# Kernel tuning notes

Hardware: AMD Instinct MI355X
Metric: run time of the kernel (lower is better)

The kernel has to match this reference:

```python
import jax, jax.numpy as jnp
import numpy as np

N_NODES = 100000
N_EDGES = 1600000
NEG_SLOPE = 0.2
EPS = 1e-16


def gat_conv(x, edge_index, W, att_src, att_dst, bias, heads, out_ch, concat):
    # x: [N, F_in]; edge_index: [2, E] with edge (src j -> dst i)
    N = x.shape[0]
    src, dst = edge_index[0], edge_index[1]
    h = (x @ W).reshape(N, heads, out_ch)              # [N, H, C]
    a_src = (h * att_src[None]).sum(-1)                # [N, H]
    a_dst = (h * att_dst[None]).sum(-1)                # [N, H]
    e = a_src[src] + a_dst[dst]                        # [E, H]
    e = jnp.where(e > 0, e, NEG_SLOPE * e)             # LeakyReLU(0.2)
    # segment softmax over destination node
    m = jax.ops.segment_max(e, dst, num_segments=N)    # [N, H]
    m = jnp.where(jnp.isfinite(m), m, 0.0)
    ex = jnp.exp(e - m[dst])                           # [E, H]
    s = jax.ops.segment_sum(ex, dst, num_segments=N)   # [N, H]
    alpha = ex / (s[dst] + EPS)                        # [E, H]
    msg = h[src] * alpha[..., None]                    # [E, H, C]
    out = jax.ops.segment_sum(msg, dst, num_segments=N)  # [N, H, C]
    if concat:
        out = out.reshape(N, heads * out_ch)
    else:
        out = out.mean(axis=1)
    return out + bias


def setup_inputs() -> dict:
    key = jax.random.key(0)
    ks = jax.random.split(key, 8)
    x = jax.random.normal(ks[0], (N_NODES, 2), dtype=jnp.float32)
    edge_index = jax.random.randint(ks[1], (2, N_EDGES), 0, N_NODES, dtype=jnp.int64)
    glorot = lambda k, shape, fan: jax.random.normal(k, shape, jnp.float32) * (1.0 / np.sqrt(fan))
    W1 = glorot(ks[2], (2, 128), 2)
    att_src1 = glorot(ks[3], (8, 16), 16)
    att_dst1 = glorot(ks[4], (8, 16), 16)
    b1 = jnp.zeros((128,), jnp.float32)
    W2 = glorot(ks[5], (128, 4), 128)
    att_src2 = glorot(ks[6], (1, 4), 4)
    att_dst2 = glorot(ks[7], (1, 4), 4)
    b2 = jnp.zeros((4,), jnp.float32)
    return {"x": x, "edge_index": edge_index, "W1": W1, "att_src1": att_src1,
            "att_dst1": att_dst1, "b1": b1, "W2": W2, "att_src2": att_src2,
            "att_dst2": att_dst2, "b2": b2}


def reference(x, edge_index, W1, att_src1, att_dst1, b1, W2, att_src2, att_dst2, b2):
    h = gat_conv(x, edge_index, W1, att_src1, att_dst1, b1, heads=8, out_ch=16, concat=True)
    h = jax.nn.relu(h)
    # dropout p=0.6 is identity in eval mode
    h = gat_conv(h, edge_index, W2, att_src2, att_dst2, b2, heads=1, out_ch=4, concat=True)
    return jax.nn.log_softmax(h, axis=1)
```

## Files before the change

kernel.cpp:

```cpp
#include <hip/hip_runtime.h>
#include <math.h>

static constexpr float kNegSlope = 0.2f;
static constexpr float kEps = 1e-16f;
static constexpr int SLICES = 256;
static constexpr int BSHIFT = 6;
static constexpr int BMASK = 63;
static constexpr unsigned SRCMASK = 0x1FFFFu;
static constexpr int CAP = 1536;

__device__ __forceinline__ float leaky(float v) {
    return v > 0.0f ? v : kNegSlope * v;
}


__global__ __launch_bounds__(512) void k_hist1(const int* __restrict__ ei,
                                               int* __restrict__ table,
                                               int* __restrict__ rowptr,
                                               int E, int N, int NBUCK) {
    __shared__ int hist[1664];
    int b = blockIdx.x, t = threadIdx.x;
    if (b == 0 && t == 0) rowptr[N] = E;
    for (int i = t; i < NBUCK; i += 512) hist[i] = 0;
    __syncthreads();
    int S = (((E + SLICES - 1) / SLICES) + 3) & ~3;
    int lo = b * S, hi = min(lo + S, E);
    for (int i = lo + t * 4; i < hi; i += 512 * 4) {
        int4 dv = *(const int4*)(ei + E + i);
        atomicAdd(&hist[dv.x >> BSHIFT], 1);
        atomicAdd(&hist[dv.y >> BSHIFT], 1);
        atomicAdd(&hist[dv.z >> BSHIFT], 1);
        atomicAdd(&hist[dv.w >> BSHIFT], 1);
    }
    __syncthreads();
    for (int i = t; i < NBUCK; i += 512) table[i * SLICES + b] = hist[i];
}

__global__ __launch_bounds__(256) void k_scan_reduce(const int* __restrict__ src,
                                                     int* __restrict__ partial, int n) {
    __shared__ int wsum[4];
    int b = blockIdx.x, t = threadIdx.x;
    int base = b * 1024 + t * 4;
    int s = 0;
#pragma unroll
    for (int k = 0; k < 4; ++k) {
        int idx = base + k;
        s += (idx < n) ? src[idx] : 0;
    }
#pragma unroll
    for (int off = 1; off < 64; off <<= 1) s += __shfl_xor(s, off);
    if ((t & 63) == 0) wsum[t >> 6] = s;
    __syncthreads();
    if (t == 0) partial[b] = wsum[0] + wsum[1] + wsum[2] + wsum[3];
}

__global__ __launch_bounds__(256) void k_scan_apply(int* __restrict__ data,
                                                    const int* __restrict__ partial,
                                                    int n, int nsb) {
    __shared__ int sm[8];
    __shared__ int baseSh;
    int b = blockIdx.x, t = threadIdx.x;
    int acc = 0;
    for (int i = t; i < b; i += 256) acc += partial[i];
#pragma unroll
    for (int off = 1; off < 64; off <<= 1) acc += __shfl_xor(acc, off);
    if ((t & 63) == 0) sm[t >> 6] = acc;
    __syncthreads();
    if (t == 0) baseSh = sm[0] + sm[1] + sm[2] + sm[3];
    __syncthreads();
    int chunkBase = baseSh;
    __syncthreads();
    int base = b * 1024 + t * 4;
    int v[4];
#pragma unroll
    for (int k = 0; k < 4; ++k) {
        int idx = base + k;
        v[k] = (idx < n) ? data[idx] : 0;
    }
    int sum4 = v[0] + v[1] + v[2] + v[3];
    int s = sum4;
#pragma unroll
    for (int off = 1; off < 64; off <<= 1) {
        int u = __shfl_up(s, off);
        if ((t & 63) >= off) s += u;
    }
    if ((t & 63) == 63) sm[t >> 6] = s;
    __syncthreads();
    int woff = 0;
    int w = t >> 6;
    for (int ww = 0; ww < w; ++ww) woff += sm[ww];
    int ex = chunkBase + woff + (s - sum4);
#pragma unroll
    for (int k = 0; k < 4; ++k) {
        int idx = base + k;
        if (idx < n) data[idx] = ex;
        ex += v[k];
    }
}

__global__ __launch_bounds__(512) void k_bin2(const int* __restrict__ ei,
                                              const int* __restrict__ table,
                                              unsigned* __restrict__ sbuf, int E, int NBUCK) {
    __shared__ int cur[1664];
    int b = blockIdx.x, t = threadIdx.x;
    for (int i = t; i < NBUCK; i += 512) cur[i] = table[i * SLICES + b];
    __syncthreads();
    int S = (((E + SLICES - 1) / SLICES) + 3) & ~3;
    int lo = b * S, hi = min(lo + S, E);
    for (int i = lo + t * 4; i < hi; i += 512 * 4) {
        int4 sv = *(const int4*)(ei + i);
        int4 dv = *(const int4*)(ei + E + i);
        int pos;
        pos = atomicAdd(&cur[dv.x >> BSHIFT], 1);
        sbuf[pos] = (unsigned)sv.x | ((unsigned)(dv.x & BMASK) << 17);
        pos = atomicAdd(&cur[dv.y >> BSHIFT], 1);
        sbuf[pos] = (unsigned)sv.y | ((unsigned)(dv.y & BMASK) << 17);
        pos = atomicAdd(&cur[dv.z >> BSHIFT], 1);
        sbuf[pos] = (unsigned)sv.z | ((unsigned)(dv.z & BMASK) << 17);
        pos = atomicAdd(&cur[dv.w >> BSHIFT], 1);
        sbuf[pos] = (unsigned)sv.w | ((unsigned)(dv.w & BMASK) << 17);
    }
}

__global__ __launch_bounds__(512, 4) void k_bfinal_g1(
        const unsigned* __restrict__ sbuf, const int* __restrict__ table,
        int* __restrict__ rowptr, int* __restrict__ ssrc,
        const float* __restrict__ x,
        const float* __restrict__ W1, const float* __restrict__ att_src1,
        const float* __restrict__ att_dst1, const float* __restrict__ b1,
        const float* __restrict__ W2, float* __restrict__ h2,
        int N, int E, int NBUCK) {
    __shared__ int hist[64];
    __shared__ int excl[64];
    __shared__ int cur[64];
    __shared__ int sl[CAP];
    __shared__ float pbuf[32];
    int b = blockIdx.x;
    int t = threadIdx.x;
    int lo = table[b * SLICES];
    int hi = (b + 1 < NBUCK) ? table[(b + 1) * SLICES] : E;
    int cnt = hi - lo;
    bool inLds = (cnt <= CAP);

    if (t < 64) hist[t] = 0;
    if (t >= 64 && t < 96) {
        int u = t - 64;
        int which = u >> 4;
        int hd = u & 15;
        int h = hd >> 1, d = hd & 1;
        const float* att = which ? att_dst1 : att_src1;
        float s = 0.0f;
#pragma unroll
        for (int c = 0; c < 16; ++c) s += W1[d * 128 + h * 16 + c] * att[h * 16 + c];
        pbuf[which * 16 + d * 8 + h] = s;
    }
    __syncthreads();

    for (int i = lo + t; i < hi; i += 512) atomicAdd(&hist[sbuf[i] >> 17], 1);
    __syncthreads();

    if (t < 64) {
        int own = hist[t];
        int v = own;
#pragma unroll
        for (int off = 1; off < 64; off <<= 1) {
            int u = __shfl_up(v, off);
            if (t >= off) v += u;
        }
        excl[t] = v - own;
        cur[t] = v - own;
        int node = (b << BSHIFT) + t;
        if (node < N) rowptr[node] = lo + (v - own);
    }
    __syncthreads();

    if (inLds) {
        for (int i = lo + t; i < hi; i += 512) {
            unsigned v = sbuf[i];
            int pos = atomicAdd(&cur[v >> 17], 1);
            sl[pos] = (int)(v & SRCMASK);
        }
        __syncthreads();
        for (int i = t; i < cnt; i += 512) ssrc[lo + i] = sl[i];
    } else {
        for (int i = lo + t; i < hi; i += 512) {
            unsigned v = sbuf[i];
            int pos = atomicAdd(&cur[v >> 17], 1);
            ssrc[lo + pos] = (int)(v & SRCMASK);
        }
        __syncthreads();
    }
    __syncthreads();

    int dl = t >> 3, q = t & 7;
    int node = (b << BSHIFT) + dl;
    int st = excl[dl];
    int ecnt = hist[dl];
    float2 xn = ((const float2*)x)[min(node, N - 1)];
    float Ps0[8], Ps1[8], adv[8], l[8], s0[8], s1[8];
#pragma unroll
    for (int h = 0; h < 8; ++h) {
        Ps0[h] = pbuf[h];
        Ps1[h] = pbuf[8 + h];
        adv[h] = xn.x * pbuf[16 + h] + xn.y * pbuf[24 + h];
        l[h] = 0.f; s0[h] = 0.f; s1[h] = 0.f;
    }
    if (inLds) {
        for (int j = q; j < ecnt; j += 8) {
            int src = sl[st + j];
            float2 xs = ((const float2*)x)[src];
#pragma unroll
            for (int h = 0; h < 8; ++h) {
                float p = __expf(leaky(xs.x * Ps0[h] + xs.y * Ps1[h] + adv[h]));
                l[h] += p; s0[h] += p * xs.x; s1[h] += p * xs.y;
            }
        }
    } else {
        for (int j = q; j < ecnt; j += 8) {
            int src = ssrc[lo + st + j];
            float2 xs = ((const float2*)x)[src];
#pragma unroll
            for (int h = 0; h < 8; ++h) {
                float p = __expf(leaky(xs.x * Ps0[h] + xs.y * Ps1[h] + adv[h]));
                l[h] += p; s0[h] += p * xs.x; s1[h] += p * xs.y;
            }
        }
    }
#pragma unroll
    for (int off = 1; off < 8; off <<= 1) {
#pragma unroll
        for (int h = 0; h < 8; ++h) {
            l[h] += __shfl_xor(l[h], off);
            s0[h] += __shfl_xor(s0[h], off);
            s1[h] += __shfl_xor(s1[h], off);
        }
    }
    float h0 = 0.f, h1v = 0.f, h2v = 0.f, h3 = 0.f;
    {
        float inv = 1.0f / (l[q] + kEps);
        float sX0 = s0[q] * inv, sX1 = s1[q] * inv;
#pragma unroll
        for (int c = 0; c < 16; ++c) {
            int col = q * 16 + c;
            float o = fmaxf(W1[col] * sX0 + W1[128 + col] * sX1 + b1[col], 0.0f);
            h0 += o * W2[col * 4 + 0];
            h1v += o * W2[col * 4 + 1];
            h2v += o * W2[col * 4 + 2];
            h3 += o * W2[col * 4 + 3];
        }
    }
#pragma unroll
    for (int off = 1; off < 8; off <<= 1) {
        h0 += __shfl_xor(h0, off);
        h1v += __shfl_xor(h1v, off);
        h2v += __shfl_xor(h2v, off);
        h3 += __shfl_xor(h3, off);
    }
    if (node < N && q == 0) {
        ((float4*)h2)[node] = make_float4(h0, h1v, h2v, h3);
    }
}

__global__ __launch_bounds__(256) void k_gather2_out(
        const int* __restrict__ rowptr, const int* __restrict__ ssrc,
        const float* __restrict__ h2, const float* __restrict__ att_src2,
        const float* __restrict__ att_dst2, const float* __restrict__ b2,
        float* __restrict__ out, int N) {
    int idx = blockIdx.x * blockDim.x + threadIdx.x;
    int n = idx >> 3, q = idx & 7;
    if (n >= N) return;
    int start = rowptr[n], end = rowptr[n + 1];
    float4 as2 = *(const float4*)att_src2;
    float4 ad2v = *(const float4*)att_dst2;
    float4 hn = ((const float4*)h2)[n];
    float ad = hn.x * ad2v.x + hn.y * ad2v.y + hn.z * ad2v.z + hn.w * ad2v.w;
    float l = 0.0f;
    float4 acc = make_float4(0.f, 0.f, 0.f, 0.f);
    for (int j = start + q; j < end; j += 8) {
        int src = ssrc[j];
        float4 hv = ((const float4*)h2)[src];
        float e = hv.x * as2.x + hv.y * as2.y + hv.z * as2.z + hv.w * as2.w + ad;
        float p = __expf(leaky(e));
        l += p;
        acc.x += p * hv.x; acc.y += p * hv.y; acc.z += p * hv.z; acc.w += p * hv.w;
    }
#pragma unroll
    for (int off = 1; off < 8; off <<= 1) {
        l += __shfl_xor(l, off);
        acc.x += __shfl_xor(acc.x, off);
        acc.y += __shfl_xor(acc.y, off);
        acc.z += __shfl_xor(acc.z, off);
        acc.w += __shfl_xor(acc.w, off);
    }
    if (q == 0) {
        float inv = 1.0f / (l + kEps);
        float4 v = make_float4(acc.x * inv + b2[0], acc.y * inv + b2[1],
                               acc.z * inv + b2[2], acc.w * inv + b2[3]);
        float mx = fmaxf(fmaxf(v.x, v.y), fmaxf(v.z, v.w));
        float sum = __expf(v.x - mx) + __expf(v.y - mx) + __expf(v.z - mx) + __expf(v.w - mx);
        float lse = mx + logf(sum);
        ((float4*)out)[n] = make_float4(v.x - lse, v.y - lse, v.z - lse, v.w - lse);
    }
}

extern "C" void kernel_launch(void* const* d_in, const int* in_sizes, int n_in,
                              void* d_out, int out_size, void* d_ws, size_t ws_size,
                              hipStream_t stream) {
    const float* x        = (const float*)d_in[0];
    const int*   ei       = (const int*)d_in[1];
    const float* W1       = (const float*)d_in[2];
    const float* att_src1 = (const float*)d_in[3];
    const float* att_dst1 = (const float*)d_in[4];
    const float* b1       = (const float*)d_in[5];
    const float* W2       = (const float*)d_in[6];
    const float* att_src2 = (const float*)d_in[7];
    const float* att_dst2 = (const float*)d_in[8];
    const float* b2       = (const float*)d_in[9];

    const int N = in_sizes[0] / 2;
    const int E = in_sizes[1] / 2;
    const int NBUCK = (N + BMASK) >> BSHIFT;
    const int ntable = NBUCK * SLICES;
    const int nsb = (ntable + 1023) / 1024;

    int* table     = (int*)d_ws;
    int* partial   = table + ntable + 64;
    int* rowptr    = partial + 1024;
    int* ssrc      = rowptr + ((N + 4) & ~3);
    unsigned* sbuf = (unsigned*)(ssrc + E);
    float* h2      = (float*)(sbuf + E);

    k_hist1<<<SLICES, 512, 0, stream>>>(ei, table, rowptr, E, N, NBUCK);
    k_scan_reduce<<<nsb, 256, 0, stream>>>(table, partial, ntable);
    k_scan_apply<<<nsb, 256, 0, stream>>>(table, partial, ntable, nsb);
    k_bin2<<<SLICES, 512, 0, stream>>>(ei, table, sbuf, E, NBUCK);

    k_bfinal_g1<<<NBUCK, 512, 0, stream>>>(sbuf, table, rowptr, ssrc, x,
                                           W1, att_src1, att_dst1, b1, W2, h2,
                                           N, E, NBUCK);

    k_gather2_out<<<(N * 8 + 255) / 256, 256, 0, stream>>>(rowptr, ssrc, h2,
                                                           att_src2, att_dst2, b2,
                                                           (float*)d_out, N);
}
```

Before: 174.3 us.

## Carry gathered source features through binning to avoid random x loads

The binning kernel now gathers each edge's source node features x[src] and writes them next to the packed src/dst word, so the per-bucket kernel reads contiguous features instead of doing random gathers. The bucket kernel stages both raw words and features in LDS, sorts them together, and reads features from LDS in the attention loop. The random gather moves into the binning pass, where it costs extra scattered 8-byte writes, and LDS use per block grows to about 30KB, which may reduce occupancy.

```diff
diff --git a/kernel.cpp b/kernel.cpp
--- a/kernel.cpp
+++ b/kernel.cpp
@@ -100,30 +100,39 @@
 
 __global__ __launch_bounds__(512) void k_bin2(const int* __restrict__ ei,
                                               const int* __restrict__ table,
-                                              unsigned* __restrict__ sbuf, int E, int NBUCK) {
+                                              const float* __restrict__ x,
+                                              unsigned* __restrict__ sbufs,
+                                              float2* __restrict__ sbufx,
+                                              int E, int NBUCK) {
     __shared__ int cur[1664];
     int b = blockIdx.x, t = threadIdx.x;
     for (int i = t; i < NBUCK; i += 512) cur[i] = table[i * SLICES + b];
     __syncthreads();
     int S = (((E + SLICES - 1) / SLICES) + 3) & ~3;
     int lo = b * S, hi = min(lo + S, E);
+    const float2* x2 = (const float2*)x;
     for (int i = lo + t * 4; i < hi; i += 512 * 4) {
         int4 sv = *(const int4*)(ei + i);
         int4 dv = *(const int4*)(ei + E + i);
         int pos;
         pos = atomicAdd(&cur[dv.x >> BSHIFT], 1);
-        sbuf[pos] = (unsigned)sv.x | ((unsigned)(dv.x & BMASK) << 17);
+        sbufs[pos] = (unsigned)sv.x | ((unsigned)(dv.x & BMASK) << 17);
+        sbufx[pos] = x2[sv.x];
         pos = atomicAdd(&cur[dv.y >> BSHIFT], 1);
-        sbuf[pos] = (unsigned)sv.y | ((unsigned)(dv.y & BMASK) << 17);
+        sbufs[pos] = (unsigned)sv.y | ((unsigned)(dv.y & BMASK) << 17);
+        sbufx[pos] = x2[sv.y];
         pos = atomicAdd(&cur[dv.z >> BSHIFT], 1);
-        sbuf[pos] = (unsigned)sv.z | ((unsigned)(dv.z & BMASK) << 17);
+        sbufs[pos] = (unsigned)sv.z | ((unsigned)(dv.z & BMASK) << 17);
+        sbufx[pos] = x2[sv.z];
         pos = atomicAdd(&cur[dv.w >> BSHIFT], 1);
-        sbuf[pos] = (unsigned)sv.w | ((unsigned)(dv.w & BMASK) << 17);
+        sbufs[pos] = (unsigned)sv.w | ((unsigned)(dv.w & BMASK) << 17);
+        sbufx[pos] = x2[sv.w];
     }
 }
 
 __global__ __launch_bounds__(512, 4) void k_bfinal_g1(
-        const unsigned* __restrict__ sbuf, const int* __restrict__ table,
+        const unsigned* __restrict__ sbufs, const float2* __restrict__ sbufx,
+        const int* __restrict__ table,
         int* __restrict__ rowptr, int* __restrict__ ssrc,
         const float* __restrict__ x,
         const float* __restrict__ W1, const float* __restrict__ att_src1,
@@ -133,7 +142,10 @@
     __shared__ int hist[64];
     __shared__ int excl[64];
     __shared__ int cur[64];
-    __shared__ int sl[CAP];
+    __shared__ unsigned raws[CAP];
+    __shared__ float2 rawx[CAP];
+    __shared__ float2 slx[CAP];
+    __shared__ int sls[CAP];
     __shared__ float pbuf[32];
     int b = blockIdx.x;
     int t = threadIdx.x;
@@ -156,7 +168,16 @@
     }
     __syncthreads();
 
-    for (int i = lo + t; i < hi; i += 512) atomicAdd(&hist[sbuf[i] >> 17], 1);
+    if (inLds) {
+        for (int i = t; i < cnt; i += 512) {
+            unsigned v = sbufs[lo + i];
+            raws[i] = v;
+            rawx[i] = sbufx[lo + i];
+            atomicAdd(&hist[v >> 17], 1);
+        }
+    } else {
+        for (int i = lo + t; i < hi; i += 512) atomicAdd(&hist[sbufs[i] >> 17], 1);
+    }
     __syncthreads();
 
     if (t < 64) {
@@ -175,16 +196,17 @@
     __syncthreads();
 
     if (inLds) {
-        for (int i = lo + t; i < hi; i += 512) {
-            unsigned v = sbuf[i];
+        for (int i = t; i < cnt; i += 512) {
+            unsigned v = raws[i];
             int pos = atomicAdd(&cur[v >> 17], 1);
-            sl[pos] = (int)(v & SRCMASK);
+            sls[pos] = (int)(v & SRCMASK);
+            slx[pos] = rawx[i];
         }
         __syncthreads();
-        for (int i = t; i < cnt; i += 512) ssrc[lo + i] = sl[i];
+        for (int i = t; i < cnt; i += 512) ssrc[lo + i] = sls[i];
     } else {
         for (int i = lo + t; i < hi; i += 512) {
-            unsigned v = sbuf[i];
+            unsigned v = sbufs[i];
             int pos = atomicAdd(&cur[v >> 17], 1);
             ssrc[lo + pos] = (int)(v & SRCMASK);
         }
@@ -207,8 +229,7 @@
     }
     if (inLds) {
         for (int j = q; j < ecnt; j += 8) {
-            int src = sl[st + j];
-            float2 xs = ((const float2*)x)[src];
+            float2 xs = slx[st + j];
 #pragma unroll
             for (int h = 0; h < 8; ++h) {
                 float p = __expf(leaky(xs.x * Ps0[h] + xs.y * Ps1[h] + adv[h]));
@@ -217,8 +238,9 @@
         }
     } else {
         for (int j = q; j < ecnt; j += 8) {
+            float2 xs = sbufx[lo + st + j];
             int src = ssrc[lo + st + j];
-            float2 xs = ((const float2*)x)[src];
+            xs = ((const float2*)x)[src];
 #pragma unroll
             for (int h = 0; h < 8; ++h) {
                 float p = __expf(leaky(xs.x * Ps0[h] + xs.y * Ps1[h] + adv[h]));
@@ -327,15 +349,16 @@
     int* partial   = table + ntable + 64;
     int* rowptr    = partial + 1024;
     int* ssrc      = rowptr + ((N + 4) & ~3);
-    unsigned* sbuf = (unsigned*)(ssrc + E);
-    float* h2      = (float*)(sbuf + E);
+    unsigned* sbufs = (unsigned*)(ssrc + E);
+    float2* sbufx  = (float2*)(sbufs + E);
+    float* h2      = (float*)(sbufx + E);
 
     k_hist1<<<SLICES, 512, 0, stream>>>(ei, table, rowptr, E, N, NBUCK);
     k_scan_reduce<<<nsb, 256, 0, stream>>>(table, partial, ntable);
     k_scan_apply<<<nsb, 256, 0, stream>>>(table, partial, ntable, nsb);
-    k_bin2<<<SLICES, 512, 0, stream>>>(ei, table, sbuf, E, NBUCK);
-
-    k_bfinal_g1<<<NBUCK, 512, 0, stream>>>(sbuf, table, rowptr, ssrc, x,
+    k_bin2<<<SLICES, 512, 0, stream>>>(ei, table, x, sbufs, sbufx, E, NBUCK);
+
+    k_bfinal_g1<<<NBUCK, 512, 0, stream>>>(sbufs, sbufx, table, rowptr, ssrc, x,
                                            W1, att_src1, att_dst1, b1, W2, h2,
                                            N, E, NBUCK);
 
```

New measurement: 197.7 us. +13.4%, slower.

## Widen destination buckets to 128 nodes and stage raw edges in LDS

Applied to the files above, without the earlier changes.

Each bucket now covers 128 destination nodes instead of 64, which halves the number of buckets and the histogram/scan table size, and doubles per-block work in the fused first-layer kernel. The raw packed edges are read from global once into LDS and reused for both the histogram and the scatter pass, rather than read twice. The prefix scan now spans two wavefronts, and each node is handled by 4 lanes instead of 8, with every lane covering two heads. The larger LDS footprint (about 23 KB per block) may lower occupancy, and fewer lanes per node mean a longer serial edge loop per lane.

```diff
diff --git a/kernel.cpp b/kernel.cpp
--- a/kernel.cpp
+++ b/kernel.cpp
@@ -4,10 +4,10 @@
 static constexpr float kNegSlope = 0.2f;
 static constexpr float kEps = 1e-16f;
 static constexpr int SLICES = 256;
-static constexpr int BSHIFT = 6;
-static constexpr int BMASK = 63;
+static constexpr int BSHIFT = 7;
+static constexpr int BMASK = 127;
 static constexpr unsigned SRCMASK = 0x1FFFFu;
-static constexpr int CAP = 1536;
+static constexpr int CAP = 2816;
 
 __device__ __forceinline__ float leaky(float v) {
     return v > 0.0f ? v : kNegSlope * v;
@@ -18,7 +18,7 @@
                                                int* __restrict__ table,
                                                int* __restrict__ rowptr,
                                                int E, int N, int NBUCK) {
-    __shared__ int hist[1664];
+    __shared__ int hist[832];
     int b = blockIdx.x, t = threadIdx.x;
     if (b == 0 && t == 0) rowptr[N] = E;
     for (int i = t; i < NBUCK; i += 512) hist[i] = 0;
@@ -101,7 +101,7 @@
 __global__ __launch_bounds__(512) void k_bin2(const int* __restrict__ ei,
                                               const int* __restrict__ table,
                                               unsigned* __restrict__ sbuf, int E, int NBUCK) {
-    __shared__ int cur[1664];
+    __shared__ int cur[832];
     int b = blockIdx.x, t = threadIdx.x;
     for (int i = t; i < NBUCK; i += 512) cur[i] = table[i * SLICES + b];
     __syncthreads();
@@ -130,10 +130,12 @@
         const float* __restrict__ att_dst1, const float* __restrict__ b1,
         const float* __restrict__ W2, float* __restrict__ h2,
         int N, int E, int NBUCK) {
-    __shared__ int hist[64];
-    __shared__ int excl[64];
-    __shared__ int cur[64];
-    __shared__ int sl[CAP];
+    __shared__ int hist[128];
+    __shared__ int sc[128];
+    __shared__ int excl[128];
+    __shared__ int cur[128];
+    __shared__ unsigned raws[CAP];
+    __shared__ int sls[CAP];
     __shared__ float pbuf[32];
     int b = blockIdx.x;
     int t = threadIdx.x;
@@ -142,9 +144,9 @@
     int cnt = hi - lo;
     bool inLds = (cnt <= CAP);
 
-    if (t < 64) hist[t] = 0;
-    if (t >= 64 && t < 96) {
-        int u = t - 64;
+    if (t < 128) hist[t] = 0;
+    if (t >= 128 && t < 160) {
+        int u = t - 128;
         int which = u >> 4;
         int hd = u & 15;
         int h = hd >> 1, d = hd & 1;
@@ -156,32 +158,46 @@
     }
     __syncthreads();
 
-    for (int i = lo + t; i < hi; i += 512) atomicAdd(&hist[sbuf[i] >> 17], 1);
-    __syncthreads();
-
-    if (t < 64) {
+    if (inLds) {
+        for (int i = t; i < cnt; i += 512) {
+            unsigned v = sbuf[lo + i];
+            raws[i] = v;
+            atomicAdd(&hist[v >> 17], 1);
+        }
+    } else {
+        for (int i = lo + t; i < hi; i += 512) atomicAdd(&hist[sbuf[i] >> 17], 1);
+    }
+    __syncthreads();
+
+    if (t < 128) {
+        int lane = t & 63;
         int own = hist[t];
         int v = own;
 #pragma unroll
         for (int off = 1; off < 64; off <<= 1) {
             int u = __shfl_up(v, off);
-            if (t >= off) v += u;
-        }
-        excl[t] = v - own;
-        cur[t] = v - own;
+            if (lane >= off) v += u;
+        }
+        sc[t] = v;
+    }
+    __syncthreads();
+    if (t < 128) {
+        int ex = sc[t] - hist[t] + (t >= 64 ? sc[63] : 0);
+        excl[t] = ex;
+        cur[t] = ex;
         int node = (b << BSHIFT) + t;
-        if (node < N) rowptr[node] = lo + (v - own);
+        if (node < N) rowptr[node] = lo + ex;
     }
     __syncthreads();
 
     if (inLds) {
-        for (int i = lo + t; i < hi; i += 512) {
-            unsigned v = sbuf[i];
+        for (int i = t; i < cnt; i += 512) {
+            unsigned v = raws[i];
             int pos = atomicAdd(&cur[v >> 17], 1);
-            sl[pos] = (int)(v & SRCMASK);
+            sls[pos] = (int)(v & SRCMASK);
         }
         __syncthreads();
-        for (int i = t; i < cnt; i += 512) ssrc[lo + i] = sl[i];
+        for (int i = t; i < cnt; i += 512) ssrc[lo + i] = sls[i];
     } else {
         for (int i = lo + t; i < hi; i += 512) {
             unsigned v = sbuf[i];
@@ -192,7 +208,7 @@
     }
     __syncthreads();
 
-    int dl = t >> 3, q = t & 7;
+    int dl = t >> 2, q = t & 3;
     int node = (b << BSHIFT) + dl;
     int st = excl[dl];
     int ecnt = hist[dl];
@@ -206,8 +222,8 @@
         l[h] = 0.f; s0[h] = 0.f; s1[h] = 0.f;
     }
     if (inLds) {
-        for (int j = q; j < ecnt; j += 8) {
-            int src = sl[st + j];
+        for (int j = q; j < ecnt; j += 4) {
+            int src = sls[st + j];
             float2 xs = ((const float2*)x)[src];
 #pragma unroll
             for (int h = 0; h < 8; ++h) {
@@ -216,7 +232,7 @@
             }
         }
     } else {
-        for (int j = q; j < ecnt; j += 8) {
+        for (int j = q; j < ecnt; j += 4) {
             int src = ssrc[lo + st + j];
             float2 xs = ((const float2*)x)[src];
 #pragma unroll
@@ -227,7 +243,7 @@
         }
     }
 #pragma unroll
-    for (int off = 1; off < 8; off <<= 1) {
+    for (int off = 1; off < 4; off <<= 1) {
 #pragma unroll
         for (int h = 0; h < 8; ++h) {
             l[h] += __shfl_xor(l[h], off);
@@ -236,12 +252,14 @@
         }
     }
     float h0 = 0.f, h1v = 0.f, h2v = 0.f, h3 = 0.f;
-    {
-        float inv = 1.0f / (l[q] + kEps);
-        float sX0 = s0[q] * inv, sX1 = s1[q] * inv;
+#pragma unroll
+    for (int k = 0; k < 2; ++k) {
+        int h = q + 4 * k;
+        float inv = 1.0f / (l[h] + kEps);
+        float sX0 = s0[h] * inv, sX1 = s1[h] * inv;
 #pragma unroll
         for (int c = 0; c < 16; ++c) {
-            int col = q * 16 + c;
+            int col = h * 16 + c;
             float o = fmaxf(W1[col] * sX0 + W1[128 + col] * sX1 + b1[col], 0.0f);
             h0 += o * W2[col * 4 + 0];
             h1v += o * W2[col * 4 + 1];
@@ -250,7 +268,7 @@
         }
     }
 #pragma unroll
-    for (int off = 1; off < 8; off <<= 1) {
+    for (int off = 1; off < 4; off <<= 1) {
         h0 += __shfl_xor(h0, off);
         h1v += __shfl_xor(h1v, off);
         h2v += __shfl_xor(h2v, off);
```

Result: faster. 168.6 us (-3.2%).
